# Performance work log

Measured on AMD Instinct MI355X. Metric: run time of the kernel, lower is better.

## Reference

```python
import jax, jax.numpy as jnp
import numpy as np

N = 100_000      # nodes
E = 1_600_000    # edges
IN, H, OUT = 128, 64, 32


def _gcn_edges(edge_index, n):
    """Add self-loops and compute symmetric GCN normalization (PyG gcn_norm)."""
    src, dst = edge_index[0], edge_index[1]
    loops = jnp.arange(n, dtype=src.dtype)
    src = jnp.concatenate([src, loops])
    dst = jnp.concatenate([dst, loops])
    deg = jax.ops.segment_sum(jnp.ones_like(dst, jnp.float32), dst, num_segments=n)
    dinv = jnp.where(deg > 0, jax.lax.rsqrt(deg), 0.0)
    norm = dinv[src] * dinv[dst]          # [E+N]
    return src, dst, norm


def _gcn_conv(x, src, dst, norm, W, b, n):
    h = x @ W.T                           # dense transform [n, out]
    msg = h[src] * norm[:, None]          # gather + scale per edge
    out = jax.ops.segment_sum(msg, dst, num_segments=n)  # scatter-add
    return out + b


def setup_inputs() -> dict:
    key = jax.random.key(0)
    k1, k2, k3, k4 = jax.random.split(key, 4)
    x = jax.random.normal(k1, (N, IN), dtype=jnp.float32)
    edge_index = jax.random.randint(k2, (2, E), 0, N, dtype=jnp.int32)
    # xavier_normal_: std = sqrt(2 / (fan_in + fan_out))
    W1 = jax.random.normal(k3, (H, IN), dtype=jnp.float32) * np.sqrt(2.0 / (IN + H))
    b1 = jnp.zeros((H,), dtype=jnp.float32)
    W2 = jax.random.normal(k4, (OUT, H), dtype=jnp.float32) * np.sqrt(2.0 / (H + OUT))
    b2 = jnp.zeros((OUT,), dtype=jnp.float32)
    return {"x": x, "edge_index": edge_index, "W1": W1, "b1": b1, "W2": W2, "b2": b2}


def reference(x, edge_index, W1, b1, W2, b2):
    n = x.shape[0]
    src, dst, norm = _gcn_edges(edge_index, n)
    h = _gcn_conv(x, src, dst, norm, W1, b1, n)
    h = jax.nn.relu(h)
    out = _gcn_conv(h, src, dst, norm, W2, b2, n)
    return out
```

## Files before the change

kernel.cpp:

```cpp
#include <hip/hip_runtime.h>

#define THREADS 256
#define G1 256
#define MAXNB 4096
#define BCAP 2688

using bf16x8 = __attribute__((ext_vector_type(8))) short;
using f32x4 = __attribute__((ext_vector_type(4))) float;

static __device__ __forceinline__ unsigned short f2bf(float f) {
  unsigned u = __float_as_uint(f);
  unsigned r = (u + 0x7fff + ((u >> 16) & 1)) >> 16;
  return (unsigned short)r;
}
static __device__ __forceinline__ float bflo(unsigned w) {
  return __uint_as_float(w << 16);
}
static __device__ __forceinline__ float bfhi(unsigned w) {
  return __uint_as_float(w & 0xffff0000u);
}
static __device__ __forceinline__ unsigned pk2(float a, float b) {
  return (unsigned)f2bf(a) | ((unsigned)f2bf(b) << 16);
}


__global__ void k_scan_chunk(const int* __restrict__ cnt, int* __restrict__ rp,
                             int* __restrict__ bsum, int m) {
  __shared__ int s[256];
  int b = blockIdx.x, t = threadIdx.x;
  int base = b * 1024 + t * 4;
  int v[4];
  int sum = 0;
#pragma unroll
  for (int k = 0; k < 4; ++k) {
    int i = base + k;
    v[k] = (i < m) ? cnt[i] : 0;
    sum += v[k];
  }
  s[t] = sum;
  __syncthreads();
  int mine = sum;
  for (int off = 1; off < 256; off <<= 1) {
    int y = (t >= off) ? s[t - off] : 0;
    __syncthreads();
    s[t] += y;
    __syncthreads();
  }
  int run = s[t] - mine;
  if (t == 255) bsum[b] = s[255];
#pragma unroll
  for (int k = 0; k < 4; ++k) {
    int i = base + k;
    if (i <= m) rp[i] = run;
    run += v[k];
  }
}

__global__ void k_scan_bsum(int* __restrict__ bsum, int nb) {
  __shared__ int s[256];
  int t = threadIdx.x;
  int v = (t < nb) ? bsum[t] : 0;
  s[t] = v;
  __syncthreads();
  for (int off = 1; off < 256; off <<= 1) {
    int y = (t >= off) ? s[t - off] : 0;
    __syncthreads();
    s[t] += y;
    __syncthreads();
  }
  if (t < nb) bsum[t] = s[t] - v;
}


__launch_bounds__(256)
__global__ void k_pcount(const int* __restrict__ dst, int* __restrict__ C, int e,
                         int NB, int chunk, unsigned* __restrict__ h1b,
                         unsigned* __restrict__ h2b, int n) {
  __shared__ int h[MAXNB];
  int blk = blockIdx.x, t = threadIdx.x;
  if (blk == 0) {
    if (t < 32) h1b[(size_t)n * 32 + t] = 0u;
    else if (t < 48) h2b[(size_t)n * 16 + (t - 32)] = 0u;
  }
  for (int i = t; i < NB; i += 256) h[i] = 0;
  __syncthreads();
  int beg = blk * chunk;
  int stop = min(e, beg + chunk);
  for (int j = beg + t; j < stop; j += 256) atomicAdd(&h[dst[j] >> 7], 1);
  __syncthreads();
  for (int i = t; i < NB; i += 256) C[i * G1 + blk] = h[i];
}

__launch_bounds__(256)
__global__ void k_partition(const int* __restrict__ src, const int* __restrict__ dst,
                            const int* __restrict__ Cs, const int* __restrict__ bsum,
                            int* __restrict__ bpack, int e, int NB, int chunk) {
  __shared__ int cur[MAXNB];
  int blk = blockIdx.x, t = threadIdx.x;
  for (int i = t; i < NB; i += 256) {
    int f = i * G1 + blk;
    cur[i] = Cs[f] + bsum[f >> 10];
  }
  __syncthreads();
  int beg = blk * chunk;
  int stop = min(e, beg + chunk);
  for (int j = beg + t; j < stop; j += 256) {
    int d = dst[j];
    int b = d >> 7;
    int pos = atomicAdd(&cur[b], 1);
    bpack[pos] = (src[j] << 7) | (d & 127);
  }
}

__launch_bounds__(256)
__global__ void k_bucket_csr(const int* __restrict__ bpack, const int* __restrict__ Cs,
                             const int* __restrict__ bsum, int* __restrict__ rp,
                             float* __restrict__ dinv, int* __restrict__ csr_src,
                             int n, int e, int NB) {
  __shared__ int cl[128];
  __shared__ int cur[128];
  __shared__ int buf[BCAP];
  int blk = blockIdx.x, t = threadIdx.x;
  int fb = blk * G1;
  int base = Cs[fb] + bsum[fb >> 10];
  int end;
  if (blk == NB - 1) {
    end = e;
  } else {
    int fe = (blk + 1) * G1;
    end = Cs[fe] + bsum[fe >> 10];
  }
  int cnt = end - base;
  if (t < 128) cl[t] = 0;
  __syncthreads();
  if (cnt <= BCAP) {
    for (int j = base + t; j < end; j += 256) {
      int p = bpack[j];
      buf[j - base] = p;
      atomicAdd(&cl[p & 127], 1);
    }
  } else {
    for (int j = base + t; j < end; j += 256) atomicAdd(&cl[bpack[j] & 127], 1);
  }
  __syncthreads();
  int own = (t < 128) ? cl[t] : 0;
  for (int off = 1; off < 128; off <<= 1) {
    int y = (t >= off && t < 128) ? cl[t - off] : 0;
    __syncthreads();
    if (t < 128) cl[t] += y;
    __syncthreads();
  }
  if (t < 128) {
    int excl = cl[t] - own;
    int v = (blk << 7) + t;
    if (v < n) {
      rp[v] = base + excl;
      dinv[v] = rsqrtf((float)own + 1.0f);
    }
    cur[t] = base + excl;
  }
  __syncthreads();
  if (cnt <= BCAP) {
    for (int j = t; j < cnt; j += 256) {
      int p = buf[j];
      int pos = atomicAdd(&cur[p & 127], 1);
      csr_src[pos] = p >> 7;
    }
  } else {
    for (int j = base + t; j < end; j += 256) {
      int p = bpack[j];
      int pos = atomicAdd(&cur[p & 127], 1);
      csr_src[pos] = p >> 7;
    }
  }
  if (blk == 0 && t == 0) rp[n] = e;
}


__launch_bounds__(256)
__global__ void k_gemm1(const float* __restrict__ x, const float* __restrict__ W1,
                        const float* __restrict__ dinv, unsigned short* __restrict__ h1b,
                        int n) {
  __shared__ uint4 sXb[64 * 16];
  __shared__ uint4 sWb[64 * 16];
  __shared__ __align__(16) unsigned short sOut[64 * 64];
  int t = threadIdx.x;
  const float4* x4 = (const float4*)x;
  const float4* W14 = (const float4*)W1;
  int rbase = blockIdx.x * 64;
#pragma unroll
  for (int p = 0; p < 4; ++p) {
    int q = t + 256 * p;
    int r = q >> 4, s = q & 15;
    int gr = rbase + r;
    float4 v0 = make_float4(0.f, 0.f, 0.f, 0.f), v1 = v0;
    if (gr < n) {
      v0 = x4[(size_t)gr * 32 + s * 2];
      v1 = x4[(size_t)gr * 32 + s * 2 + 1];
    }
    uint4 pk;
    pk.x = pk2(v0.x, v0.y);
    pk.y = pk2(v0.z, v0.w);
    pk.z = pk2(v1.x, v1.y);
    pk.w = pk2(v1.z, v1.w);
    sXb[r * 16 + (s ^ (r & 15))] = pk;
  }
#pragma unroll
  for (int p = 0; p < 4; ++p) {
    int q = t + 256 * p;
    int c = q >> 4, s = q & 15;
    float4 v0 = W14[c * 32 + s * 2];
    float4 v1 = W14[c * 32 + s * 2 + 1];
    uint4 pk;
    pk.x = pk2(v0.x, v0.y);
    pk.y = pk2(v0.z, v0.w);
    pk.z = pk2(v1.x, v1.y);
    pk.w = pk2(v1.z, v1.w);
    sWb[c * 16 + (s ^ (c & 15))] = pk;
  }
  __syncthreads();
  int lane = t & 63;
  int w = t >> 6;
  int l16 = lane & 15, quad = lane >> 4;
  int arow = w * 16 + l16;
  f32x4 acc0 = {0.f, 0.f, 0.f, 0.f};
  f32x4 acc1 = {0.f, 0.f, 0.f, 0.f};
  f32x4 acc2 = {0.f, 0.f, 0.f, 0.f};
  f32x4 acc3 = {0.f, 0.f, 0.f, 0.f};
#pragma unroll
  for (int kc = 0; kc < 4; ++kc) {
    int slot = kc * 4 + quad;
    uint4 ua = sXb[arow * 16 + (slot ^ (arow & 15))];
    bf16x8 a = *(bf16x8*)&ua;
    uint4 ub0 = sWb[(0 + l16) * 16 + (slot ^ l16)];
    uint4 ub1 = sWb[(16 + l16) * 16 + (slot ^ l16)];
    uint4 ub2 = sWb[(32 + l16) * 16 + (slot ^ l16)];
    uint4 ub3 = sWb[(48 + l16) * 16 + (slot ^ l16)];
    acc0 = __builtin_amdgcn_mfma_f32_16x16x32_bf16(a, *(bf16x8*)&ub0, acc0, 0, 0, 0);
    acc1 = __builtin_amdgcn_mfma_f32_16x16x32_bf16(a, *(bf16x8*)&ub1, acc1, 0, 0, 0);
    acc2 = __builtin_amdgcn_mfma_f32_16x16x32_bf16(a, *(bf16x8*)&ub2, acc2, 0, 0, 0);
    acc3 = __builtin_amdgcn_mfma_f32_16x16x32_bf16(a, *(bf16x8*)&ub3, acc3, 0, 0, 0);
  }
  float dvr[4];
#pragma unroll
  for (int r = 0; r < 4; ++r) {
    int grow = rbase + w * 16 + quad * 4 + r;
    dvr[r] = (grow < n) ? dinv[grow] : 0.f;
  }
#pragma unroll
  for (int r = 0; r < 4; ++r) {
    int rl = w * 16 + quad * 4 + r;
    sOut[rl * 64 + 0 + l16] = f2bf(acc0[r] * dvr[r]);
    sOut[rl * 64 + 16 + l16] = f2bf(acc1[r] * dvr[r]);
    sOut[rl * 64 + 32 + l16] = f2bf(acc2[r] * dvr[r]);
    sOut[rl * 64 + 48 + l16] = f2bf(acc3[r] * dvr[r]);
  }
  __syncthreads();
#pragma unroll
  for (int p = 0; p < 2; ++p) {
    int q = t + 256 * p;
    int r = q >> 3, s = q & 7;
    int gr = rbase + r;
    if (gr < n)
      *(uint4*)&h1b[(size_t)gr * 64 + s * 8] = *(uint4*)&sOut[r * 64 + s * 8];
  }
}


__launch_bounds__(256)
__global__ void k_agg1(const unsigned* __restrict__ h1p, const float* __restrict__ dinv,
                       const int* __restrict__ rp, const int* __restrict__ csr_src,
                       unsigned* __restrict__ agg1b, int n) {
  int gid = blockIdx.x * 256 + threadIdx.x;
  int v = gid >> 4, f4 = gid & 15;
  if (v >= n) return;
  const uint2* h1q = (const uint2*)h1p;
  int beg = rp[v], end = rp[v + 1];
  uint2 w0 = h1q[(size_t)v * 16 + f4];
  float acc[8][4];
#pragma unroll
  for (int k = 0; k < 8; ++k)
#pragma unroll
    for (int c = 0; c < 4; ++c) acc[k][c] = 0.f;
  acc[0][0] = bflo(w0.x);
  acc[0][1] = bfhi(w0.x);
  acc[0][2] = bflo(w0.y);
  acc[0][3] = bfhi(w0.y);
  for (int j = beg; j < end; j += 8) {
    int s[8];
#pragma unroll
    for (int k = 0; k < 8; ++k) s[k] = csr_src[j + k];
#pragma unroll
    for (int k = 1; k < 8; ++k) s[k] = (j + k < end) ? s[k] : n;
    uint2 g[8];
#pragma unroll
    for (int k = 0; k < 8; ++k) g[k] = h1q[(size_t)s[k] * 16 + f4];
#pragma unroll
    for (int k = 0; k < 8; ++k) {
      acc[k][0] += bflo(g[k].x);
      acc[k][1] += bfhi(g[k].x);
      acc[k][2] += bflo(g[k].y);
      acc[k][3] += bfhi(g[k].y);
    }
  }
  float s0 = ((acc[0][0] + acc[1][0]) + (acc[2][0] + acc[3][0])) +
             ((acc[4][0] + acc[5][0]) + (acc[6][0] + acc[7][0]));
  float s1 = ((acc[0][1] + acc[1][1]) + (acc[2][1] + acc[3][1])) +
             ((acc[4][1] + acc[5][1]) + (acc[6][1] + acc[7][1]));
  float s2 = ((acc[0][2] + acc[1][2]) + (acc[2][2] + acc[3][2])) +
             ((acc[4][2] + acc[5][2]) + (acc[6][2] + acc[7][2]));
  float s3 = ((acc[0][3] + acc[1][3]) + (acc[2][3] + acc[3][3])) +
             ((acc[4][3] + acc[5][3]) + (acc[6][3] + acc[7][3]));
  float dv = dinv[v];
  uint2 o;
  o.x = pk2(dv * s0, dv * s1);
  o.y = pk2(dv * s2, dv * s3);
  ((uint2*)agg1b)[(size_t)v * 16 + f4] = o;
}


__launch_bounds__(256)
__global__ void k_gemm2(const unsigned* __restrict__ agg1b, const float* __restrict__ b1,
                        const float* __restrict__ W2, const float* __restrict__ dinv,
                        unsigned short* __restrict__ h2b, int n) {
  __shared__ uint4 sXb[64 * 8];
  __shared__ uint4 sWb[32 * 8];
  __shared__ __align__(16) unsigned short sOut[64 * 32];
  int t = threadIdx.x;
  int rbase = blockIdx.x * 64;
  const uint4* a4 = (const uint4*)agg1b;
  const float4* b14 = (const float4*)b1;
  const float4* W24 = (const float4*)W2;
#pragma unroll
  for (int p = 0; p < 2; ++p) {
    int q = t + 256 * p;
    int r = q >> 3, s = q & 7;
    int gr = rbase + r;
    uint4 o = make_uint4(0u, 0u, 0u, 0u);
    if (gr < n) {
      uint4 a = a4[(size_t)gr * 8 + s];
      float4 blo = b14[s * 2], bhi = b14[s * 2 + 1];
      o.x = pk2(fmaxf(bflo(a.x) + blo.x, 0.f), fmaxf(bfhi(a.x) + blo.y, 0.f));
      o.y = pk2(fmaxf(bflo(a.y) + blo.z, 0.f), fmaxf(bfhi(a.y) + blo.w, 0.f));
      o.z = pk2(fmaxf(bflo(a.z) + bhi.x, 0.f), fmaxf(bfhi(a.z) + bhi.y, 0.f));
      o.w = pk2(fmaxf(bflo(a.w) + bhi.z, 0.f), fmaxf(bfhi(a.w) + bhi.w, 0.f));
    }
    sXb[r * 8 + (s ^ (r & 7))] = o;
  }
  {
    int c = t >> 3, s = t & 7;
    float4 v0 = W24[c * 16 + s * 2];
    float4 v1 = W24[c * 16 + s * 2 + 1];
    uint4 pk;
    pk.x = pk2(v0.x, v0.y);
    pk.y = pk2(v0.z, v0.w);
    pk.z = pk2(v1.x, v1.y);
    pk.w = pk2(v1.z, v1.w);
    sWb[c * 8 + (s ^ (c & 7))] = pk;
  }
  __syncthreads();
  int lane = t & 63;
  int w = t >> 6;
  int l16 = lane & 15, quad = lane >> 4;
  int arow = w * 16 + l16;
  f32x4 acc0 = {0.f, 0.f, 0.f, 0.f};
  f32x4 acc1 = {0.f, 0.f, 0.f, 0.f};
#pragma unroll
  for (int kc = 0; kc < 2; ++kc) {
    int slot = kc * 4 + quad;
    uint4 ua = sXb[arow * 8 + (slot ^ (arow & 7))];
    bf16x8 a = *(bf16x8*)&ua;
    uint4 ub0 = sWb[l16 * 8 + (slot ^ (l16 & 7))];
    uint4 ub1 = sWb[(16 + l16) * 8 + (slot ^ (l16 & 7))];
    acc0 = __builtin_amdgcn_mfma_f32_16x16x32_bf16(a, *(bf16x8*)&ub0, acc0, 0, 0, 0);
    acc1 = __builtin_amdgcn_mfma_f32_16x16x32_bf16(a, *(bf16x8*)&ub1, acc1, 0, 0, 0);
  }
  float dvr[4];
#pragma unroll
  for (int r = 0; r < 4; ++r) {
    int grow = rbase + w * 16 + quad * 4 + r;
    dvr[r] = (grow < n) ? dinv[grow] : 0.f;
  }
#pragma unroll
  for (int r = 0; r < 4; ++r) {
    int rl = w * 16 + quad * 4 + r;
    sOut[rl * 32 + l16] = f2bf(acc0[r] * dvr[r]);
    sOut[rl * 32 + 16 + l16] = f2bf(acc1[r] * dvr[r]);
  }
  __syncthreads();
  {
    int r = t >> 2, s = t & 3;
    int gr = rbase + r;
    if (gr < n)
      *(uint4*)&h2b[(size_t)gr * 32 + s * 8] = *(uint4*)&sOut[r * 32 + s * 8];
  }
}


__launch_bounds__(256)
__global__ void k_agg2(const unsigned* __restrict__ h2p, const float* __restrict__ dinv,
                       const int* __restrict__ rp, const int* __restrict__ csr_src,
                       const float* __restrict__ b2, float* __restrict__ out, int n) {
  int gid = blockIdx.x * 256 + threadIdx.x;
  int v = gid >> 3, f4 = gid & 7;
  if (v >= n) return;
  const uint2* h2q = (const uint2*)h2p;
  int beg = rp[v], end = rp[v + 1];
  uint2 w0 = h2q[(size_t)v * 8 + f4];
  float acc[8][4];
#pragma unroll
  for (int k = 0; k < 8; ++k)
#pragma unroll
    for (int c = 0; c < 4; ++c) acc[k][c] = 0.f;
  acc[0][0] = bflo(w0.x);
  acc[0][1] = bfhi(w0.x);
  acc[0][2] = bflo(w0.y);
  acc[0][3] = bfhi(w0.y);
  for (int j = beg; j < end; j += 8) {
    int s[8];
#pragma unroll
    for (int k = 0; k < 8; ++k) s[k] = csr_src[j + k];
#pragma unroll
    for (int k = 1; k < 8; ++k) s[k] = (j + k < end) ? s[k] : n;
    uint2 g[8];
#pragma unroll
    for (int k = 0; k < 8; ++k) g[k] = h2q[(size_t)s[k] * 8 + f4];
#pragma unroll
    for (int k = 0; k < 8; ++k) {
      acc[k][0] += bflo(g[k].x);
      acc[k][1] += bfhi(g[k].x);
      acc[k][2] += bflo(g[k].y);
      acc[k][3] += bfhi(g[k].y);
    }
  }
  float s0 = ((acc[0][0] + acc[1][0]) + (acc[2][0] + acc[3][0])) +
             ((acc[4][0] + acc[5][0]) + (acc[6][0] + acc[7][0]));
  float s1 = ((acc[0][1] + acc[1][1]) + (acc[2][1] + acc[3][1])) +
             ((acc[4][1] + acc[5][1]) + (acc[6][1] + acc[7][1]));
  float s2 = ((acc[0][2] + acc[1][2]) + (acc[2][2] + acc[3][2])) +
             ((acc[4][2] + acc[5][2]) + (acc[6][2] + acc[7][2]));
  float s3 = ((acc[0][3] + acc[1][3]) + (acc[2][3] + acc[3][3])) +
             ((acc[4][3] + acc[5][3]) + (acc[6][3] + acc[7][3]));
  float dv = dinv[v];
  float4 bv = ((const float4*)b2)[f4];
  float4 o;
  o.x = fmaf(dv, s0, bv.x);
  o.y = fmaf(dv, s1, bv.y);
  o.z = fmaf(dv, s2, bv.z);
  o.w = fmaf(dv, s3, bv.w);
  ((float4*)out)[(size_t)v * 8 + f4] = o;
}


extern "C" void kernel_launch(void* const* d_in, const int* in_sizes, int n_in,
                              void* d_out, int out_size, void* d_ws, size_t ws_size,
                              hipStream_t stream) {
  const float* x = (const float*)d_in[0];
  const int* ei = (const int*)d_in[1];
  const float* W1 = (const float*)d_in[2];
  const float* b1 = (const float*)d_in[3];
  const float* W2 = (const float*)d_in[4];
  const float* b2 = (const float*)d_in[5];
  float* out = (float*)d_out;

  const int n = in_sizes[0] / 128;
  const int e = in_sizes[1] / 2;
  const int* src = ei;
  const int* dst = ei + e;

  const int NB = (n + 127) >> 7;
  const int m = NB * G1;
  const int chunk = (e + G1 - 1) / G1;
  const int NC = (m + 1 + 1023) / 1024;

  char* base = (char*)d_ws;
  size_t off = 0;
  auto alloc = [&](size_t bytes) {
    char* p = base + off;
    off = (off + bytes + 255) & ~(size_t)255;
    return p;
  };
  int* C = (int*)alloc((size_t)m * 4);
  int* Cs = (int*)alloc((size_t)(m + 1) * 4);
  int* bsum = (int*)alloc(1024 * 4);
  int* bpack = (int*)alloc((size_t)e * 4);
  int* rp = (int*)alloc((size_t)(n + 1) * 4);
  int* csr_src = (int*)alloc((size_t)(e + 8) * 4);
  float* dinv = (float*)alloc((size_t)n * 4);
  unsigned short* h1b = (unsigned short*)alloc((size_t)(n + 1) * 64 * 2);
  unsigned* agg1b = (unsigned*)alloc((size_t)n * 64 * 2);
  unsigned short* h2b = (unsigned short*)alloc((size_t)(n + 1) * 32 * 2);

  k_pcount<<<G1, 256, 0, stream>>>(dst, C, e, NB, chunk, (unsigned*)h1b,
                                   (unsigned*)h2b, n);
  k_scan_chunk<<<NC, 256, 0, stream>>>(C, Cs, bsum, m);
  k_scan_bsum<<<1, 256, 0, stream>>>(bsum, NC);
  k_partition<<<G1, 256, 0, stream>>>(src, dst, Cs, bsum, bpack, e, NB, chunk);
  k_bucket_csr<<<NB, 256, 0, stream>>>(bpack, Cs, bsum, rp, dinv, csr_src, n, e, NB);

  k_gemm1<<<(n + 63) / 64, 256, 0, stream>>>(x, W1, dinv, h1b, n);
  {
    long long total = (long long)n * 16;
    k_agg1<<<(int)((total + 255) / 256), 256, 0, stream>>>((const unsigned*)h1b, dinv,
                                                           rp, csr_src, agg1b, n);
  }

  k_gemm2<<<(n + 63) / 64, 256, 0, stream>>>(agg1b, b1, W2, dinv, h2b, n);
  {
    long long total = (long long)n * 8;
    k_agg2<<<(int)((total + 255) / 256), 256, 0, stream>>>((const unsigned*)h2b, dinv,
                                                           rp, csr_src, b2, out, n);
  }
}
```

Measured before the change: 209.7 us.

## Fuse layer-1 aggregation into layer-2 GEMM and drop the bsum scan kernel

```diff
diff --git a/kernel.cpp b/kernel.cpp
--- a/kernel.cpp
+++ b/kernel.cpp
@@ -54,21 +54,6 @@
     if (i <= m) rp[i] = run;
     run += v[k];
   }
-}
-
-__global__ void k_scan_bsum(int* __restrict__ bsum, int nb) {
-  __shared__ int s[256];
-  int t = threadIdx.x;
-  int v = (t < nb) ? bsum[t] : 0;
-  s[t] = v;
-  __syncthreads();
-  for (int off = 1; off < 256; off <<= 1) {
-    int y = (t >= off) ? s[t - off] : 0;
-    __syncthreads();
-    s[t] += y;
-    __syncthreads();
-  }
-  if (t < nb) bsum[t] = s[t] - v;
 }
 
 
@@ -94,12 +79,43 @@
 __launch_bounds__(256)
 __global__ void k_partition(const int* __restrict__ src, const int* __restrict__ dst,
                             const int* __restrict__ Cs, const int* __restrict__ bsum,
-                            int* __restrict__ bpack, int e, int NB, int chunk) {
+                            int* __restrict__ bpack, int e, int NB, int chunk,
+                            int NC) {
   __shared__ int cur[MAXNB];
+  __shared__ int sb[1024];
+  __shared__ int ss[256];
   int blk = blockIdx.x, t = threadIdx.x;
+  {
+    int b4 = t * 4;
+    int v4[4];
+    int sum = 0;
+#pragma unroll
+    for (int k = 0; k < 4; ++k) {
+      int i = b4 + k;
+      v4[k] = (i < NC) ? bsum[i] : 0;
+      sum += v4[k];
+    }
+    ss[t] = sum;
+    __syncthreads();
+    int mine = sum;
+    for (int off = 1; off < 256; off <<= 1) {
+      int y = (t >= off) ? ss[t - off] : 0;
+      __syncthreads();
+      ss[t] += y;
+      __syncthreads();
+    }
+    int run = ss[t] - mine;
+#pragma unroll
+    for (int k = 0; k < 4; ++k) {
+      int i = b4 + k;
+      if (i < 1024) sb[i] = run;
+      run += v4[k];
+    }
+    __syncthreads();
+  }
   for (int i = t; i < NB; i += 256) {
     int f = i * G1 + blk;
-    cur[i] = Cs[f] + bsum[f >> 10];
+    cur[i] = Cs[f] + sb[f >> 10];
   }
   __syncthreads();
   int beg = blk * chunk;
@@ -116,23 +132,52 @@
 __global__ void k_bucket_csr(const int* __restrict__ bpack, const int* __restrict__ Cs,
                              const int* __restrict__ bsum, int* __restrict__ rp,
                              float* __restrict__ dinv, int* __restrict__ csr_src,
-                             int n, int e, int NB) {
+                             int n, int e, int NB, int NC) {
   __shared__ int cl[128];
   __shared__ int cur[128];
   __shared__ int buf[BCAP];
+  __shared__ int sb[1024];
+  __shared__ int ss[256];
   int blk = blockIdx.x, t = threadIdx.x;
+  {
+    int b4 = t * 4;
+    int v4[4];
+    int sum = 0;
+#pragma unroll
+    for (int k = 0; k < 4; ++k) {
+      int i = b4 + k;
+      v4[k] = (i < NC) ? bsum[i] : 0;
+      sum += v4[k];
+    }
+    ss[t] = sum;
+    __syncthreads();
+    int mine = sum;
+    for (int off = 1; off < 256; off <<= 1) {
+      int y = (t >= off) ? ss[t - off] : 0;
+      __syncthreads();
+      ss[t] += y;
+      __syncthreads();
+    }
+    int run = ss[t] - mine;
+#pragma unroll
+    for (int k = 0; k < 4; ++k) {
+      int i = b4 + k;
+      if (i < 1024) sb[i] = run;
+      run += v4[k];
+    }
+  }
   int fb = blk * G1;
-  int base = Cs[fb] + bsum[fb >> 10];
-  int end;
+  int base, end;
+  if (t < 128) cl[t] = 0;
+  __syncthreads();
+  base = Cs[fb] + sb[fb >> 10];
   if (blk == NB - 1) {
     end = e;
   } else {
     int fe = (blk + 1) * G1;
-    end = Cs[fe] + bsum[fe >> 10];
+    end = Cs[fe] + sb[fe >> 10];
   }
   int cnt = end - base;
-  if (t < 128) cl[t] = 0;
-  __syncthreads();
   if (cnt <= BCAP) {
     for (int j = base + t; j < end; j += 256) {
       int p = bpack[j];
@@ -268,95 +313,81 @@
 
 
 __launch_bounds__(256)
-__global__ void k_agg1(const unsigned* __restrict__ h1p, const float* __restrict__ dinv,
-                       const int* __restrict__ rp, const int* __restrict__ csr_src,
-                       unsigned* __restrict__ agg1b, int n) {
-  int gid = blockIdx.x * 256 + threadIdx.x;
-  int v = gid >> 4, f4 = gid & 15;
-  if (v >= n) return;
-  const uint2* h1q = (const uint2*)h1p;
-  int beg = rp[v], end = rp[v + 1];
-  uint2 w0 = h1q[(size_t)v * 16 + f4];
-  float acc[8][4];
-#pragma unroll
-  for (int k = 0; k < 8; ++k)
-#pragma unroll
-    for (int c = 0; c < 4; ++c) acc[k][c] = 0.f;
-  acc[0][0] = bflo(w0.x);
-  acc[0][1] = bfhi(w0.x);
-  acc[0][2] = bflo(w0.y);
-  acc[0][3] = bfhi(w0.y);
-  for (int j = beg; j < end; j += 8) {
-    int s[8];
-#pragma unroll
-    for (int k = 0; k < 8; ++k) s[k] = csr_src[j + k];
-#pragma unroll
-    for (int k = 1; k < 8; ++k) s[k] = (j + k < end) ? s[k] : n;
-    uint2 g[8];
-#pragma unroll
-    for (int k = 0; k < 8; ++k) g[k] = h1q[(size_t)s[k] * 16 + f4];
-#pragma unroll
-    for (int k = 0; k < 8; ++k) {
-      acc[k][0] += bflo(g[k].x);
-      acc[k][1] += bfhi(g[k].x);
-      acc[k][2] += bflo(g[k].y);
-      acc[k][3] += bfhi(g[k].y);
-    }
-  }
-  float s0 = ((acc[0][0] + acc[1][0]) + (acc[2][0] + acc[3][0])) +
-             ((acc[4][0] + acc[5][0]) + (acc[6][0] + acc[7][0]));
-  float s1 = ((acc[0][1] + acc[1][1]) + (acc[2][1] + acc[3][1])) +
-             ((acc[4][1] + acc[5][1]) + (acc[6][1] + acc[7][1]));
-  float s2 = ((acc[0][2] + acc[1][2]) + (acc[2][2] + acc[3][2])) +
-             ((acc[4][2] + acc[5][2]) + (acc[6][2] + acc[7][2]));
-  float s3 = ((acc[0][3] + acc[1][3]) + (acc[2][3] + acc[3][3])) +
-             ((acc[4][3] + acc[5][3]) + (acc[6][3] + acc[7][3]));
-  float dv = dinv[v];
-  uint2 o;
-  o.x = pk2(dv * s0, dv * s1);
-  o.y = pk2(dv * s2, dv * s3);
-  ((uint2*)agg1b)[(size_t)v * 16 + f4] = o;
-}
-
-
-__launch_bounds__(256)
-__global__ void k_gemm2(const unsigned* __restrict__ agg1b, const float* __restrict__ b1,
+__global__ void k_fused(const unsigned* __restrict__ h1p, const float* __restrict__ b1,
                         const float* __restrict__ W2, const float* __restrict__ dinv,
+                        const int* __restrict__ rp, const int* __restrict__ csr_src,
                         unsigned short* __restrict__ h2b, int n) {
-  __shared__ uint4 sXb[64 * 8];
-  __shared__ uint4 sWb[32 * 8];
-  __shared__ __align__(16) unsigned short sOut[64 * 32];
+  __shared__ uint4 sXb2[64 * 8];
+  __shared__ uint4 sWb2[32 * 8];
+  __shared__ __align__(16) unsigned short sOut2[64 * 32];
   int t = threadIdx.x;
   int rbase = blockIdx.x * 64;
-  const uint4* a4 = (const uint4*)agg1b;
+  const uint2* h1q = (const uint2*)h1p;
+  const float4* W24 = (const float4*)W2;
   const float4* b14 = (const float4*)b1;
-  const float4* W24 = (const float4*)W2;
-#pragma unroll
-  for (int p = 0; p < 2; ++p) {
-    int q = t + 256 * p;
-    int r = q >> 3, s = q & 7;
-    int gr = rbase + r;
-    uint4 o = make_uint4(0u, 0u, 0u, 0u);
-    if (gr < n) {
-      uint4 a = a4[(size_t)gr * 8 + s];
-      float4 blo = b14[s * 2], bhi = b14[s * 2 + 1];
-      o.x = pk2(fmaxf(bflo(a.x) + blo.x, 0.f), fmaxf(bfhi(a.x) + blo.y, 0.f));
-      o.y = pk2(fmaxf(bflo(a.y) + blo.z, 0.f), fmaxf(bfhi(a.y) + blo.w, 0.f));
-      o.z = pk2(fmaxf(bflo(a.z) + bhi.x, 0.f), fmaxf(bfhi(a.z) + bhi.y, 0.f));
-      o.w = pk2(fmaxf(bflo(a.w) + bhi.z, 0.f), fmaxf(bfhi(a.w) + bhi.w, 0.f));
-    }
-    sXb[r * 8 + (s ^ (r & 7))] = o;
-  }
   {
-    int c = t >> 3, s = t & 7;
-    float4 v0 = W24[c * 16 + s * 2];
-    float4 v1 = W24[c * 16 + s * 2 + 1];
+    int c = t >> 3, s2 = t & 7;
+    float4 v0 = W24[c * 16 + s2 * 2];
+    float4 v1 = W24[c * 16 + s2 * 2 + 1];
     uint4 pk;
     pk.x = pk2(v0.x, v0.y);
     pk.y = pk2(v0.z, v0.w);
     pk.z = pk2(v1.x, v1.y);
     pk.w = pk2(v1.z, v1.w);
-    sWb[c * 8 + (s ^ (c & 7))] = pk;
+    sWb2[c * 8 + (s2 ^ (c & 7))] = pk;
+  }
+  int f4 = t & 15;
+  int rloc = t >> 4;
+#pragma unroll
+  for (int sub = 0; sub < 4; ++sub) {
+    int r = sub * 16 + rloc;
+    int v = rbase + r;
+    float r0 = 0.f, r1 = 0.f, r2 = 0.f, r3 = 0.f;
+    if (v < n) {
+      int beg = rp[v], end = rp[v + 1];
+      uint2 w0 = h1q[(size_t)v * 16 + f4];
+      float acc[4][4];
+#pragma unroll
+      for (int k = 0; k < 4; ++k)
+#pragma unroll
+        for (int c = 0; c < 4; ++c) acc[k][c] = 0.f;
+      acc[0][0] = bflo(w0.x);
+      acc[0][1] = bfhi(w0.x);
+      acc[0][2] = bflo(w0.y);
+      acc[0][3] = bfhi(w0.y);
+      for (int j = beg; j < end; j += 4) {
+        int s[4];
+#pragma unroll
+        for (int k = 0; k < 4; ++k) s[k] = csr_src[j + k];
+#pragma unroll
+        for (int k = 1; k < 4; ++k) s[k] = (j + k < end) ? s[k] : n;
+        uint2 g[4];
+#pragma unroll
+        for (int k = 0; k < 4; ++k) g[k] = h1q[(size_t)s[k] * 16 + f4];
+#pragma unroll
+        for (int k = 0; k < 4; ++k) {
+          acc[k][0] += bflo(g[k].x);
+          acc[k][1] += bfhi(g[k].x);
+          acc[k][2] += bflo(g[k].y);
+          acc[k][3] += bfhi(g[k].y);
+        }
+      }
+      float s0 = (acc[0][0] + acc[1][0]) + (acc[2][0] + acc[3][0]);
+      float s1 = (acc[0][1] + acc[1][1]) + (acc[2][1] + acc[3][1]);
+      float s2 = (acc[0][2] + acc[1][2]) + (acc[2][2] + acc[3][2]);
+      float s3 = (acc[0][3] + acc[1][3]) + (acc[2][3] + acc[3][3]);
+      float dv = dinv[v];
+      float4 bb = b14[f4];
+      r0 = fmaxf(fmaf(dv, s0, bb.x), 0.f);
+      r1 = fmaxf(fmaf(dv, s1, bb.y), 0.f);
+      r2 = fmaxf(fmaf(dv, s2, bb.z), 0.f);
+      r3 = fmaxf(fmaf(dv, s3, bb.w), 0.f);
+    }
+    unsigned u0 = pk2(r0, r1), u1 = pk2(r2, r3);
+    unsigned* xb = (unsigned*)sXb2;
+    int slot = (f4 >> 1) ^ (r & 7);
+    xb[(r * 8 + slot) * 4 + (f4 & 1) * 2 + 0] = u0;
+    xb[(r * 8 + slot) * 4 + (f4 & 1) * 2 + 1] = u1;
   }
   __syncthreads();
   int lane = t & 63;
@@ -368,10 +399,10 @@
 #pragma unroll
   for (int kc = 0; kc < 2; ++kc) {
     int slot = kc * 4 + quad;
-    uint4 ua = sXb[arow * 8 + (slot ^ (arow & 7))];
+    uint4 ua = sXb2[arow * 8 + (slot ^ (arow & 7))];
     bf16x8 a = *(bf16x8*)&ua;
-    uint4 ub0 = sWb[l16 * 8 + (slot ^ (l16 & 7))];
-    uint4 ub1 = sWb[(16 + l16) * 8 + (slot ^ (l16 & 7))];
+    uint4 ub0 = sWb2[l16 * 8 + (slot ^ (l16 & 7))];
+    uint4 ub1 = sWb2[(16 + l16) * 8 + (slot ^ (l16 & 7))];
     acc0 = __builtin_amdgcn_mfma_f32_16x16x32_bf16(a, *(bf16x8*)&ub0, acc0, 0, 0, 0);
     acc1 = __builtin_amdgcn_mfma_f32_16x16x32_bf16(a, *(bf16x8*)&ub1, acc1, 0, 0, 0);
   }
@@ -384,15 +415,15 @@
 #pragma unroll
   for (int r = 0; r < 4; ++r) {
     int rl = w * 16 + quad * 4 + r;
-    sOut[rl * 32 + l16] = f2bf(acc0[r] * dvr[r]);
-    sOut[rl * 32 + 16 + l16] = f2bf(acc1[r] * dvr[r]);
+    sOut2[rl * 32 + l16] = f2bf(acc0[r] * dvr[r]);
+    sOut2[rl * 32 + 16 + l16] = f2bf(acc1[r] * dvr[r]);
   }
   __syncthreads();
   {
-    int r = t >> 2, s = t & 3;
+    int r = t >> 2, s2 = t & 3;
     int gr = rbase + r;
     if (gr < n)
-      *(uint4*)&h2b[(size_t)gr * 32 + s * 8] = *(uint4*)&sOut[r * 32 + s * 8];
+      *(uint4*)&h2b[(size_t)gr * 32 + s2 * 8] = *(uint4*)&sOut2[r * 32 + s2 * 8];
   }
 }
 
@@ -427,20 +458,16 @@
     for (int k = 0; k < 8; ++k) g[k] = h2q[(size_t)s[k] * 8 + f4];
 #pragma unroll
     for (int k = 0; k < 8; ++k) {
-      acc[k][0] += bflo(g[k].x);
-      acc[k][1] += bfhi(g[k].x);
-      acc[k][2] += bflo(g[k].y);
-      acc[k][3] += bfhi(g[k].y);
-    }
-  }
-  float s0 = ((acc[0][0] + acc[1][0]) + (acc[2][0] + acc[3][0])) +
-             ((acc[4][0] + acc[5][0]) + (acc[6][0] + acc[7][0]));
-  float s1 = ((acc[0][1] + acc[1][1]) + (acc[2][1] + acc[3][1])) +
-             ((acc[4][1] + acc[5][1]) + (acc[6][1] + acc[7][1]));
-  float s2 = ((acc[0][2] + acc[1][2]) + (acc[2][2] + acc[3][2])) +
-             ((acc[4][2] + acc[5][2]) + (acc[6][2] + acc[7][2]));
-  float s3 = ((acc[0][3] + acc[1][3]) + (acc[2][3] + acc[3][3])) +
-             ((acc[4][3] + acc[5][3]) + (acc[6][3] + acc[7][3]));
+      acc[k & 3][0] += bflo(g[k].x);
+      acc[k & 3][1] += bfhi(g[k].x);
+      acc[k & 3][2] += bflo(g[k].y);
+      acc[k & 3][3] += bfhi(g[k].y);
+    }
+  }
+  float s0 = (acc[0][0] + acc[1][0]) + (acc[2][0] + acc[3][0]);
+  float s1 = (acc[0][1] + acc[1][1]) + (acc[2][1] + acc[3][1]);
+  float s2 = (acc[0][2] + acc[1][2]) + (acc[2][2] + acc[3][2]);
+  float s3 = (acc[0][3] + acc[1][3]) + (acc[2][3] + acc[3][3]);
   float dv = dinv[v];
   float4 bv = ((const float4*)b2)[f4];
   float4 o;
@@ -488,24 +515,18 @@
   int* csr_src = (int*)alloc((size_t)(e + 8) * 4);
   float* dinv = (float*)alloc((size_t)n * 4);
   unsigned short* h1b = (unsigned short*)alloc((size_t)(n + 1) * 64 * 2);
-  unsigned* agg1b = (unsigned*)alloc((size_t)n * 64 * 2);
   unsigned short* h2b = (unsigned short*)alloc((size_t)(n + 1) * 32 * 2);
 
   k_pcount<<<G1, 256, 0, stream>>>(dst, C, e, NB, chunk, (unsigned*)h1b,
                                    (unsigned*)h2b, n);
   k_scan_chunk<<<NC, 256, 0, stream>>>(C, Cs, bsum, m);
-  k_scan_bsum<<<1, 256, 0, stream>>>(bsum, NC);
-  k_partition<<<G1, 256, 0, stream>>>(src, dst, Cs, bsum, bpack, e, NB, chunk);
-  k_bucket_csr<<<NB, 256, 0, stream>>>(bpack, Cs, bsum, rp, dinv, csr_src, n, e, NB);
+  k_partition<<<G1, 256, 0, stream>>>(src, dst, Cs, bsum, bpack, e, NB, chunk, NC);
+  k_bucket_csr<<<NB, 256, 0, stream>>>(bpack, Cs, bsum, rp, dinv, csr_src, n, e, NB,
+                                       NC);
 
   k_gemm1<<<(n + 63) / 64, 256, 0, stream>>>(x, W1, dinv, h1b, n);
-  {
-    long long total = (long long)n * 16;
-    k_agg1<<<(int)((total + 255) / 256), 256, 0, stream>>>((const unsigned*)h1b, dinv,
-                                                           rp, csr_src, agg1b, n);
-  }
-
-  k_gemm2<<<(n + 63) / 64, 256, 0, stream>>>(agg1b, b1, W2, dinv, h2b, n);
+  k_fused<<<(n + 63) / 64, 256, 0, stream>>>((const unsigned*)h1b, b1, W2, dinv, rp,
+                                             csr_src, h2b, n);
   {
     long long total = (long long)n * 8;
     k_agg2<<<(int)((total + 255) / 256), 256, 0, stream>>>((const unsigned*)h2b, dinv,
```

New measurement: 205.2 us. 1.02x faster.
